# Kernel optimization log

Hardware: AMD Instinct MI355X
Metric: run time of the kernel (lower is better)

## Reference

```python
import jax, jax.numpy as jnp
import numpy as np

N = 50000
E = 200000
DIMS = [3, 64, 64, 64, 128, 1024, 512, 256, 2]  # hard-coded layer widths from __init__


def setup_inputs() -> dict:
    key = jax.random.key(0)
    ks = jax.random.split(key, 2 + 2 * 8)
    inp = {}
    inp["x"] = jax.random.normal(ks[0], (N, DIMS[0]), dtype=jnp.float32)
    inp["edge_index"] = jax.random.randint(ks[1], (2, E), 0, N, dtype=jnp.int32)
    for i in range(8):
        w = jax.random.normal(ks[2 + 2 * i], (DIMS[i], DIMS[i + 1]), dtype=jnp.float32) / np.sqrt(DIMS[i]).astype(np.float32)
        b = jax.random.normal(ks[3 + 2 * i], (DIMS[i + 1],), dtype=jnp.float32) * 0.01
        inp[f"W{i}"] = w
        inp[f"b{i}"] = b
    return inp


def _gcn_layer(x, row, col, norm, W, b, n):
    # PyG GCNConv: h = x @ W; out_i = sum_{j->i} norm_ij * h_j; out += b
    h = x @ W                          # [N, F_out]
    msg = h[row] * norm[:, None]       # [E+N, F_out] gather + scale
    out = jax.ops.segment_sum(msg, col, num_segments=n)  # scatter-add
    return out + b


def reference(x, edge_index, W0, b0, W1, b1, W2, b2, W3, b3, W4, b4, W5, b5, W6, b6, W7, b7):
    n = x.shape[0]
    # add self-loops (GCNConv default add_self_loops=True)
    loops = jnp.arange(n, dtype=edge_index.dtype)
    row = jnp.concatenate([edge_index[0], loops])  # source nodes
    col = jnp.concatenate([edge_index[1], loops])  # target nodes
    # symmetric degree normalization: deg counts incoming edges at col
    deg = jax.ops.segment_sum(jnp.ones_like(col, dtype=x.dtype), col, num_segments=n)
    dis = jnp.where(deg > 0, jax.lax.rsqrt(jnp.maximum(deg, 1e-12)), 0.0)
    norm = dis[row] * dis[col]  # [E+N]

    Ws = [W0, W1, W2, W3, W4, W5, W6, W7]
    bs = [b0, b1, b2, b3, b4, b5, b6, b7]
    # dropout is identity in eval mode (training=False)
    for i in range(7):
        x = jax.nn.relu(_gcn_layer(x, row, col, norm, Ws[i], bs[i], n))
    x = _gcn_layer(x, row, col, norm, Ws[7], bs[7], n)
    return x
```

## Files before the change

### kernel.cpp

```cpp
#include <hip/hip_runtime.h>
#include <hip/hip_bf16.h>

typedef __hip_bfloat16 bf16;
typedef __attribute__((ext_vector_type(8))) short short8;
typedef __attribute__((ext_vector_type(4))) float floatx4;

__device__ inline float ldf(const float* p, size_t i) { return p[i]; }
__device__ inline float ldf(const bf16* p, size_t i) { return (float)p[i]; }
__device__ inline void stf(float* p, size_t i, float v) { p[i] = v; }
__device__ inline void stf(bf16* p, size_t i, float v) { p[i] = (bf16)v; }

__device__ inline void async16(const bf16* g, bf16* l) {
    __builtin_amdgcn_global_load_lds(
        (const __attribute__((address_space(1))) void*)g,
        (__attribute__((address_space(3))) void*)l, 16, 0, 0);
}

__device__ inline void loadvec(const float* __restrict__ p, float* d) {
    float4 v = *(const float4*)p;
    d[0] = v.x; d[1] = v.y; d[2] = v.z; d[3] = v.w;
}
__device__ inline void loadvec(const bf16* __restrict__ p, float* d) {
    uint4 u = *(const uint4*)p;
    const unsigned* w = (const unsigned*)&u;
    #pragma unroll
    for (int j = 0; j < 4; ++j) {
        d[2 * j]     = __uint_as_float(w[j] << 16);
        d[2 * j + 1] = __uint_as_float(w[j] & 0xffff0000u);
    }
}
template <int VEC, typename TOut>
__device__ inline void storevec(TOut* __restrict__ p, const float* d) {
    if constexpr (sizeof(TOut) == 4) {
        #pragma unroll
        for (int j = 0; j < VEC; j += 4) {
            float4 v = {d[j], d[j + 1], d[j + 2], d[j + 3]};
            *(float4*)(p + j) = v;
        }
    } else {
        unsigned w[VEC / 2];
        #pragma unroll
        for (int j = 0; j < VEC / 2; ++j) {
            bf16 lo = (bf16)d[2 * j], hi = (bf16)d[2 * j + 1];
            w[j] = ((unsigned)*(unsigned short*)&hi << 16) | (unsigned)*(unsigned short*)&lo;
        }
        if constexpr (VEC == 8) *(uint4*)p = *(uint4*)&w[0];
        else                    *(uint2*)p = *(uint2*)&w[0];
    }
}

__global__ void detect_dtype_kernel(const unsigned short* __restrict__ x, int* __restrict__ flag) {
    __shared__ float s[256];
    float m = 0.0f;
    for (int i = threadIdx.x; i < 512; i += 256) {
        unsigned int u = ((unsigned int)x[i]) << 16;
        float v = __uint_as_float(u);
        if (!isnan(v)) m = fmaxf(m, fabsf(v));
    }
    s[threadIdx.x] = m;
    __syncthreads();
    for (int o = 128; o > 0; o >>= 1) {
        if (threadIdx.x < (unsigned)o) s[threadIdx.x] = fmaxf(s[threadIdx.x], s[threadIdx.x + o]);
        __syncthreads();
    }
    if (threadIdx.x == 0) flag[0] = (s[0] > 1e3f) ? 0 : 1;
}

struct CvtJobs {
    const void* src[14];
    float* dst[14];
    int off[15];
    int cnt;
};
__global__ void cvt_fused_kernel(CvtJobs j, const int* __restrict__ flag) {
    int t = blockIdx.x * 256 + threadIdx.x;
    if (t >= j.off[j.cnt]) return;
    int k = 0;
    while (t >= j.off[k + 1]) ++k;
    int e = t - j.off[k];
    float v = *flag ? (float)((const bf16*)j.src[k])[e] : ((const float*)j.src[k])[e];
    j.dst[k][e] = v;
}

struct WtJobs {
    const void* src[3];
    bf16* dst[3];
    int K[3], N[3];
    int off[4];
};
__global__ void wt_fused_kernel(WtJobs j, const int* __restrict__ flag) {
    int t = blockIdx.x * 256 + threadIdx.x;
    if (t >= j.off[3]) return;
    int k_ = 0;
    while (t >= j.off[k_ + 1]) ++k_;
    int e = t - j.off[k_];
    int K = j.K[k_], Nn = j.N[k_];
    int n = e / K, kk = e % K;
    size_t si = (size_t)kk * Nn + n;
    float v = *flag ? (float)((const bf16*)j.src[k_])[si] : ((const float*)j.src[k_])[si];
    j.dst[k_][e] = (bf16)v;
}

__global__ void out_kernel(const float* __restrict__ in, void* __restrict__ out,
                           int n, const int* __restrict__ flag) {
    int i = blockIdx.x * blockDim.x + threadIdx.x;
    if (i >= n) return;
    if (*flag) ((bf16*)out)[i] = (bf16)in[i];
    else       ((float*)out)[i] = in[i];
}

__global__ void zero_int_kernel(int* a, int n) {
    int i = blockIdx.x * blockDim.x + threadIdx.x;
    if (i < n) a[i] = 0;
}

__global__ void hist_kernel(const int* __restrict__ col, int* __restrict__ counts, int E) {
    int e = blockIdx.x * blockDim.x + threadIdx.x;
    if (e < E) atomicAdd(&counts[col[e]], 1);
}

__global__ void scan_reduce_kernel(const int* __restrict__ counts, int* __restrict__ bs, int n) {
    __shared__ int s[1024];
    int i = blockIdx.x * 1024 + threadIdx.x;
    s[threadIdx.x] = (i < n) ? counts[i] : 0;
    __syncthreads();
    for (int o = 512; o > 0; o >>= 1) {
        if (threadIdx.x < (unsigned)o) s[threadIdx.x] += s[threadIdx.x + o];
        __syncthreads();
    }
    if (threadIdx.x == 0) bs[blockIdx.x] = s[0];
}

__global__ void scan_blocksums_kernel(int* __restrict__ bs, int nb) {
    __shared__ int s[1024];
    int v = (threadIdx.x < (unsigned)nb) ? bs[threadIdx.x] : 0;
    s[threadIdx.x] = v;
    __syncthreads();
    for (int off = 1; off < 1024; off <<= 1) {
        int t = (threadIdx.x >= (unsigned)off) ? s[threadIdx.x - off] : 0;
        __syncthreads();
        s[threadIdx.x] += t;
        __syncthreads();
    }
    if (threadIdx.x < (unsigned)nb) bs[threadIdx.x] = s[threadIdx.x] - v;
}

__global__ void scan_final_kernel(int* __restrict__ counts, const int* __restrict__ bs,
                                  int* __restrict__ offsets, float* __restrict__ dis, int n) {
    __shared__ int s[1024];
    int i = blockIdx.x * 1024 + threadIdx.x;
    int v = (i < n) ? counts[i] : 0;
    if (i < n) { dis[i] = rsqrtf((float)(v + 1)); counts[i] = 0; }
    s[threadIdx.x] = v;
    __syncthreads();
    for (int off = 1; off < 1024; off <<= 1) {
        int t = (threadIdx.x >= (unsigned)off) ? s[threadIdx.x - off] : 0;
        __syncthreads();
        s[threadIdx.x] += t;
        __syncthreads();
    }
    if (i < n) offsets[i + 1] = s[threadIdx.x] + bs[blockIdx.x];
    if (i == 0) offsets[0] = 0;
}

__global__ void fill_kernel(const int* __restrict__ row, const int* __restrict__ col,
                            const int* __restrict__ offsets, int* __restrict__ cursor,
                            int* __restrict__ csr_src, int E) {
    int e = blockIdx.x * blockDim.x + threadIdx.x;
    if (e < E) {
        int d = col[e];
        int pos = offsets[d] + atomicAdd(&cursor[d], 1);
        csr_src[pos] = row[e];
    }
}

template <typename TIn, typename TOut>
__global__ void agg_kernel(const TIn* __restrict__ h, const int* __restrict__ offsets,
                           const int* __restrict__ csr_src, const float* __restrict__ dis,
                           const float* __restrict__ bias, TOut* __restrict__ out,
                           int n, int F, int add_bias, int relu) {
    long long idx = (long long)blockIdx.x * blockDim.x + threadIdx.x;
    long long total = (long long)n * F;
    if (idx >= total) return;
    int i = (int)(idx / F);
    int f = (int)(idx % F);
    float di = dis[i];
    float acc = di * ldf(h, (size_t)i * F + f);
    int e0 = offsets[i], e1 = offsets[i + 1];
    for (int e = e0; e < e1; ++e) {
        int s = csr_src[e];
        acc += dis[s] * ldf(h, (size_t)s * F + f);
    }
    acc *= di;
    if (add_bias) acc += bias[f];
    if (relu) acc = fmaxf(acc, 0.0f);
    stf(out, (size_t)idx, acc);
}

template <int F, int DO_BIAS, int DO_RELU, typename TIn, typename TOut>
__global__ __launch_bounds__(256) void agg_vec_kernel(
        const TIn* __restrict__ h, const int* __restrict__ offsets,
        const int* __restrict__ csr_src, const float* __restrict__ dis,
        const float* __restrict__ bias, TOut* __restrict__ out, int n) {
    constexpr int VEC = 16 / sizeof(TIn);
    constexpr int CPL = F / VEC;
    int t = blockIdx.x * 256 + threadIdx.x;
    if (t >= n * CPL) return;
    int i = t / CPL;
    int c = t % CPL;
    int fbase = c * VEC;
    float di = dis[i];
    float acc[VEC];
    loadvec(h + (size_t)i * F + fbase, acc);
    #pragma unroll
    for (int v = 0; v < VEC; ++v) acc[v] *= di;
    int e0 = offsets[i], e1 = offsets[i + 1];
    for (int e = e0; e < e1; ++e) {
        int s = csr_src[e];
        float dsv = dis[s];
        float tmp[VEC];
        loadvec(h + (size_t)s * F + fbase, tmp);
        #pragma unroll
        for (int v = 0; v < VEC; ++v) acc[v] += dsv * tmp[v];
    }
    #pragma unroll
    for (int v = 0; v < VEC; ++v) {
        acc[v] *= di;
        if (DO_BIAS) acc[v] += bias[fbase + v];
        if (DO_RELU) acc[v] = fmaxf(acc[v], 0.0f);
    }
    storevec<VEC>(out + (size_t)i * F + fbase, acc);
}

template <typename TIn, typename TOut>
__global__ void gemm_naive_kernel(const TIn* __restrict__ A, const float* __restrict__ W,
                                  const float* __restrict__ bias, TOut* __restrict__ C,
                                  int M, int Nc, int K, int add_bias, int relu) {
    long long idx = (long long)blockIdx.x * blockDim.x + threadIdx.x;
    long long total = (long long)M * Nc;
    if (idx >= total) return;
    int m = (int)(idx / Nc);
    int nc = (int)(idx % Nc);
    float acc = 0.0f;
    for (int k = 0; k < K; ++k)
        acc += ldf(A, (size_t)m * K + k) * W[(size_t)k * Nc + nc];
    if (add_bias) acc += bias[nc];
    if (relu) acc = fmaxf(acc, 0.0f);
    stf(C, (size_t)idx, acc);
}

#define TM 64
#define TN 64
#define TK 16
template <typename TIn, typename TOut>
__global__ __launch_bounds__(256) void gemm_tiled_kernel(
        const TIn* __restrict__ A, const float* __restrict__ W,
        const float* __restrict__ bias, TOut* __restrict__ C,
        int M, int Nc, int K, int add_bias, int relu) {
    __shared__ float As[TK][TM + 1];
    __shared__ float Bs[TK][TN + 1];
    int bm = blockIdx.x * TM;
    int bn = blockIdx.y * TN;
    int tid = threadIdx.x;
    int tm = (tid >> 4) << 2;
    int tn = (tid & 15) << 2;
    float acc[4][4] = {};
    for (int k0 = 0; k0 < K; k0 += TK) {
        #pragma unroll
        for (int l = 0; l < 4; ++l) {
            int idx = tid + l * 256;
            int m = idx >> 4;
            int k = idx & 15;
            int gm = bm + m;
            As[k][m] = (gm < M) ? ldf(A, (size_t)gm * K + k0 + k) : 0.0f;
        }
        #pragma unroll
        for (int l = 0; l < 4; ++l) {
            int idx = tid + l * 256;
            int k = idx >> 6;
            int nn = idx & 63;
            Bs[k][nn] = W[(size_t)(k0 + k) * Nc + bn + nn];
        }
        __syncthreads();
        #pragma unroll
        for (int k = 0; k < TK; ++k) {
            float a[4], b[4];
            #pragma unroll
            for (int i = 0; i < 4; ++i) a[i] = As[k][tm + i];
            #pragma unroll
            for (int j = 0; j < 4; ++j) b[j] = Bs[k][tn + j];
            #pragma unroll
            for (int i = 0; i < 4; ++i)
                #pragma unroll
                for (int j = 0; j < 4; ++j) acc[i][j] += a[i] * b[j];
        }
        __syncthreads();
    }
    #pragma unroll
    for (int i = 0; i < 4; ++i) {
        int gm = bm + tm + i;
        if (gm >= M) continue;
        #pragma unroll
        for (int j = 0; j < 4; ++j) {
            int gn = bn + tn + j;
            float v = acc[i][j];
            if (add_bias) v += bias[gn];
            if (relu) v = fmaxf(v, 0.0f);
            stf(C, (size_t)gm * Nc + gn, v);
        }
    }
}

template <int DO_BIAS, int DO_RELU, typename TOut>
__global__ __launch_bounds__(256) void gemm_mfma_kernel(
        const bf16* __restrict__ A,
        const bf16* __restrict__ Bt,
        const float* __restrict__ bias,
        TOut* __restrict__ C,
        int M, int Nc, int K) {
    __shared__ bf16 As[2][128 * 32];
    __shared__ bf16 Bs[2][128 * 32];
    const int tid  = threadIdx.x;
    const int wave = tid >> 6;
    const int lane = tid & 63;

    const int nwg  = (int)gridDim.x;
    const int orig = (int)blockIdx.x;
    const int q = nwg >> 3, r = nwg & 7;
    const int xcd = orig & 7;
    const int lin = orig >> 3;
    const int swz = (xcd < r ? xcd * (q + 1) : r * (q + 1) + (xcd - r) * q) + lin;
    const int nbn = Nc >> 7;
    const int bm = (swz / nbn) * 128;
    const int bn = (swz % nbn) * 128;

    const int wr = (wave >> 1) * 64;
    const int wc = (wave & 1) * 64;
    const int fm = lane & 15;
    const int fq = lane >> 4;
    const int fk = fq * 8;

    const int e0 = tid * 8;
    const int r0 = e0 >> 5, c0 = e0 & 31;
    const int e1 = (256 + tid) * 8;
    const int r1 = e1 >> 5, c1 = e1 & 31;
    int gmA0 = bm + r0; if (gmA0 > M - 1) gmA0 = M - 1;
    int gmA1 = bm + r1; if (gmA1 > M - 1) gmA1 = M - 1;

    const bf16* a0p = A  + (size_t)gmA0 * K + c0;
    const bf16* a1p = A  + (size_t)gmA1 * K + c1;
    const bf16* b0p = Bt + (size_t)(bn + r0) * K + c0;
    const bf16* b1p = Bt + (size_t)(bn + r1) * K + c1;

    floatx4 acc[4][4] = {};
    const int nt = K >> 5;

    async16(a0p, &As[0][e0]);
    async16(a1p, &As[0][e1]);
    async16(b0p, &Bs[0][e0]);
    async16(b1p, &Bs[0][e1]);

    for (int t = 0; t < nt; ++t) {
        __syncthreads();
        const int cur = t & 1;
        if (t + 1 < nt) {
            const int k0 = (t + 1) << 5;
            async16(a0p + k0, &As[cur ^ 1][e0]);
            async16(a1p + k0, &As[cur ^ 1][e1]);
            async16(b0p + k0, &Bs[cur ^ 1][e0]);
            async16(b1p + k0, &Bs[cur ^ 1][e1]);
        }
        short8 af[4], bfv[4];
        #pragma unroll
        for (int t4 = 0; t4 < 4; ++t4) {
            af[t4]  = *(const short8*)(&As[cur][(wr + t4 * 16 + fm) * 32 + fk]);
            bfv[t4] = *(const short8*)(&Bs[cur][(wc + t4 * 16 + fm) * 32 + fk]);
        }
        #pragma unroll
        for (int mt = 0; mt < 4; ++mt)
            #pragma unroll
            for (int ntc = 0; ntc < 4; ++ntc)
                acc[mt][ntc] = __builtin_amdgcn_mfma_f32_16x16x32_bf16(
                    af[mt], bfv[ntc], acc[mt][ntc], 0, 0, 0);
    }

    #pragma unroll
    for (int mt = 0; mt < 4; ++mt) {
        #pragma unroll
        for (int r2 = 0; r2 < 4; ++r2) {
            int gm = bm + wr + mt * 16 + fq * 4 + r2;
            if (gm >= M) continue;
            #pragma unroll
            for (int ntc = 0; ntc < 4; ++ntc) {
                int gn = bn + wc + ntc * 16 + fm;
                float v = acc[mt][ntc][r2];
                if (DO_BIAS) v += bias[gn];
                if (DO_RELU) v = fmaxf(v, 0.0f);
                stf(C, (size_t)gm * Nc + gn, v);
            }
        }
    }
}


static inline int cdiv(long long a, int b) { return (int)((a + b - 1) / b); }

extern "C" void kernel_launch(void* const* d_in, const int* in_sizes, int n_in,
                              void* d_out, int out_size, void* d_ws, size_t ws_size,
                              hipStream_t stream) {
    const int N = in_sizes[0] / 3;
    const int E = in_sizes[1] / 2;

    const int* edge_index = (const int*)d_in[1];
    const int* row = edge_index;
    const int* col = edge_index + E;

    char* p = (char*)d_ws;
    auto alloc = [&](size_t bytes) {
        void* r = (void*)p;
        p += (bytes + 255) & ~(size_t)255;
        return r;
    };
    void* bufA    = alloc((size_t)N * 2048);
    void* bufB    = alloc((size_t)N * 1024);
    float* dis    = (float*)alloc((size_t)N * sizeof(float));
    int* offsets  = (int*)alloc((size_t)(N + 1) * sizeof(int));
    int* cursor   = (int*)alloc((size_t)N * sizeof(int));
    int* csr_src  = (int*)alloc((size_t)E * sizeof(int));
    int* flag     = (int*)alloc(256);
    int* blocksums = (int*)alloc((size_t)cdiv(N, 1024) * sizeof(int));
    const int WfL[5] = {0, 1, 2, 3, 7};
    float* Wf[8] = {};
    float* bf_[8];
    for (int t = 0; t < 5; ++t) {
        int L = WfL[t];
        Wf[L] = (float*)alloc((size_t)in_sizes[2 + 2 * L] * sizeof(float));
    }
    for (int L = 0; L < 8; ++L)
        bf_[L] = (float*)alloc((size_t)in_sizes[3 + 2 * L] * sizeof(float));
    bf16* Wt4 = (bf16*)alloc((size_t)128 * 1024 * sizeof(bf16));
    bf16* Wt5 = (bf16*)alloc((size_t)1024 * 512 * sizeof(bf16));
    bf16* Wt6 = (bf16*)alloc((size_t)512 * 256 * sizeof(bf16));
    size_t needed = (size_t)(p - (char*)d_ws);
    if (ws_size < needed) return;

    float* fA = (float*)bufA;  bf16* hA = (bf16*)bufA;
    float* fB = (float*)bufB;  bf16* hB = (bf16*)bufB;

    const int T = 256;

    detect_dtype_kernel<<<1, 256, 0, stream>>>((const unsigned short*)d_in[0], flag);

    {
        CvtJobs cj{};
        int idx = 0, cum = 0;
        auto add = [&](const void* s, float* d, int n) {
            cj.src[idx] = s; cj.dst[idx] = d; cj.off[idx] = cum; cum += n; ++idx;
        };
        add(d_in[0], fA, N * 3);
        for (int t = 0; t < 5; ++t) {
            int L = WfL[t];
            add(d_in[2 + 2 * L], Wf[L], in_sizes[2 + 2 * L]);
        }
        for (int L = 0; L < 8; ++L)
            add(d_in[3 + 2 * L], bf_[L], in_sizes[3 + 2 * L]);
        cj.off[idx] = cum; cj.cnt = idx;
        cvt_fused_kernel<<<cdiv(cum, T), T, 0, stream>>>(cj, flag);
    }

    {
        WtJobs wj{};
        wj.src[0] = d_in[2 + 2 * 4]; wj.dst[0] = Wt4; wj.K[0] = 128;  wj.N[0] = 1024;
        wj.src[1] = d_in[2 + 2 * 5]; wj.dst[1] = Wt5; wj.K[1] = 1024; wj.N[1] = 512;
        wj.src[2] = d_in[2 + 2 * 6]; wj.dst[2] = Wt6; wj.K[2] = 512;  wj.N[2] = 256;
        wj.off[0] = 0;
        wj.off[1] = 128 * 1024;
        wj.off[2] = 128 * 1024 + 1024 * 512;
        wj.off[3] = 128 * 1024 + 1024 * 512 + 512 * 256;
        wt_fused_kernel<<<cdiv(wj.off[3], T), T, 0, stream>>>(wj, flag);
    }

    {
        zero_int_kernel<<<cdiv(N, T), T, 0, stream>>>(cursor, N);
        hist_kernel<<<cdiv(E, T), T, 0, stream>>>(col, cursor, E);
        int nb = cdiv(N, 1024);
        scan_reduce_kernel<<<nb, 1024, 0, stream>>>(cursor, blocksums, N);
        scan_blocksums_kernel<<<1, 1024, 0, stream>>>(blocksums, nb);
        scan_final_kernel<<<nb, 1024, 0, stream>>>(cursor, blocksums, offsets, dis, N);
        fill_kernel<<<cdiv(E, T), T, 0, stream>>>(row, col, offsets, cursor, csr_src, E);
    }


    agg_kernel<float, float><<<cdiv((long long)N * 3, T), T, 0, stream>>>(
        fA, offsets, csr_src, dis, nullptr, fB, N, 3, 0, 0);
    gemm_naive_kernel<float, float><<<cdiv((long long)N * 64, T), T, 0, stream>>>(
        fB, Wf[0], bf_[0], fA, N, 64, 3, 1, 1);

    {
        dim3 g(cdiv(N, TM), 64 / TN);
        gemm_tiled_kernel<float, float><<<g, 256, 0, stream>>>(fA, Wf[1], nullptr, fB, N, 64, 64, 0, 0);
        agg_vec_kernel<64, 1, 1, float, float><<<cdiv((long long)N * 16, T), T, 0, stream>>>(
            fB, offsets, csr_src, dis, bf_[1], fA, N);
    }

    {
        dim3 g(cdiv(N, TM), 64 / TN);
        gemm_tiled_kernel<float, float><<<g, 256, 0, stream>>>(fA, Wf[2], nullptr, fB, N, 64, 64, 0, 0);
        agg_vec_kernel<64, 1, 1, float, float><<<cdiv((long long)N * 16, T), T, 0, stream>>>(
            fB, offsets, csr_src, dis, bf_[2], fA, N);
    }

    {
        agg_vec_kernel<64, 0, 0, float, float><<<cdiv((long long)N * 16, T), T, 0, stream>>>(
            fA, offsets, csr_src, dis, nullptr, fB, N);
        dim3 g(cdiv(N, TM), 128 / TN);
        gemm_tiled_kernel<float, bf16><<<g, 256, 0, stream>>>(fB, Wf[3], bf_[3], hA, N, 128, 64, 1, 1);
    }

    {
        agg_vec_kernel<128, 0, 0, bf16, bf16><<<cdiv((long long)N * 16, T), T, 0, stream>>>(
            hA, offsets, csr_src, dis, nullptr, hB, N);
        int nwg = cdiv(N, 128) * (1024 / 128);
        gemm_mfma_kernel<1, 1, bf16><<<nwg, 256, 0, stream>>>(hB, Wt4, bf_[4], hA, N, 1024, 128);
    }

    {
        int nwg = cdiv(N, 128) * (512 / 128);
        gemm_mfma_kernel<0, 0, bf16><<<nwg, 256, 0, stream>>>(hA, Wt5, nullptr, hB, N, 512, 1024);
        agg_vec_kernel<512, 1, 1, bf16, bf16><<<cdiv((long long)N * 64, T), T, 0, stream>>>(
            hB, offsets, csr_src, dis, bf_[5], hA, N);
    }

    {
        int nwg = cdiv(N, 128) * (256 / 128);
        gemm_mfma_kernel<0, 0, bf16><<<nwg, 256, 0, stream>>>(hA, Wt6, nullptr, hB, N, 256, 512);
        agg_vec_kernel<256, 1, 1, bf16, bf16><<<cdiv((long long)N * 32, T), T, 0, stream>>>(
            hB, offsets, csr_src, dis, bf_[6], hA, N);
    }

    {
        gemm_naive_kernel<bf16, float><<<cdiv((long long)N * 2, T), T, 0, stream>>>(
            hA, Wf[7], nullptr, fB, N, 2, 256, 0, 0);
        agg_kernel<float, float><<<cdiv((long long)N * 2, T), T, 0, stream>>>(
            fB, offsets, csr_src, dis, bf_[7], fA, N, 2, 1, 0);
    }

    out_kernel<<<cdiv((long long)N * 2, T), T, 0, stream>>>(fA, d_out, N * 2, flag);
}
```

Measured before the change: 565.9 us.

## Triple-buffer MFMA GEMM LDS tiles and XOR-swizzle layout to avoid bank conflicts

```diff
diff --git a/kernel.cpp b/kernel.cpp
--- a/kernel.cpp
+++ b/kernel.cpp
@@ -318,8 +318,8 @@
         const float* __restrict__ bias,
         TOut* __restrict__ C,
         int M, int Nc, int K) {
-    __shared__ bf16 As[2][128 * 32];
-    __shared__ bf16 Bs[2][128 * 32];
+    __shared__ bf16 As[3][128 * 32];
+    __shared__ bf16 Bs[3][128 * 32];
     const int tid  = threadIdx.x;
     const int wave = tid >> 6;
     const int lane = tid & 63;
@@ -338,43 +338,50 @@
     const int wc = (wave & 1) * 64;
     const int fm = lane & 15;
     const int fq = lane >> 4;
-    const int fk = fq * 8;
-
+    const int fks = (fq ^ ((fm >> 1) & 3)) << 3;
+
+    const int r0 = tid >> 2;
+    const int r1 = (256 + tid) >> 2;
+    const int sc0 = ((tid & 3) ^ ((r0 >> 1) & 3)) << 3;
+    const int sc1 = (((256 + tid) & 3) ^ ((r1 >> 1) & 3)) << 3;
     const int e0 = tid * 8;
-    const int r0 = e0 >> 5, c0 = e0 & 31;
     const int e1 = (256 + tid) * 8;
-    const int r1 = e1 >> 5, c1 = e1 & 31;
     int gmA0 = bm + r0; if (gmA0 > M - 1) gmA0 = M - 1;
     int gmA1 = bm + r1; if (gmA1 > M - 1) gmA1 = M - 1;
 
-    const bf16* a0p = A  + (size_t)gmA0 * K + c0;
-    const bf16* a1p = A  + (size_t)gmA1 * K + c1;
-    const bf16* b0p = Bt + (size_t)(bn + r0) * K + c0;
-    const bf16* b1p = Bt + (size_t)(bn + r1) * K + c1;
+    const bf16* a0p = A  + (size_t)gmA0 * K + sc0;
+    const bf16* a1p = A  + (size_t)gmA1 * K + sc1;
+    const bf16* b0p = Bt + (size_t)(bn + r0) * K + sc0;
+    const bf16* b1p = Bt + (size_t)(bn + r1) * K + sc1;
+
+    auto stage = [&](int slot, int kt) {
+        const int k0 = kt << 5;
+        async16(a0p + k0, &As[slot][e0]);
+        async16(a1p + k0, &As[slot][e1]);
+        async16(b0p + k0, &Bs[slot][e0]);
+        async16(b1p + k0, &Bs[slot][e1]);
+    };
 
     floatx4 acc[4][4] = {};
     const int nt = K >> 5;
 
-    async16(a0p, &As[0][e0]);
-    async16(a1p, &As[0][e1]);
-    async16(b0p, &Bs[0][e0]);
-    async16(b1p, &Bs[0][e1]);
-
+    stage(0, 0);
+    if (nt > 1) stage(1, 1);
+
+    int cur = 0;
     for (int t = 0; t < nt; ++t) {
-        __syncthreads();
-        const int cur = t & 1;
-        if (t + 1 < nt) {
-            const int k0 = (t + 1) << 5;
-            async16(a0p + k0, &As[cur ^ 1][e0]);
-            async16(a1p + k0, &As[cur ^ 1][e1]);
-            async16(b0p + k0, &Bs[cur ^ 1][e0]);
-            async16(b1p + k0, &Bs[cur ^ 1][e1]);
+        if (t + 1 < nt) asm volatile("s_waitcnt vmcnt(4)" ::: "memory");
+        else            asm volatile("s_waitcnt vmcnt(0)" ::: "memory");
+        __builtin_amdgcn_s_barrier();
+        if (t + 2 < nt) {
+            int sp = cur + 2; if (sp >= 3) sp -= 3;
+            stage(sp, t + 2);
         }
         short8 af[4], bfv[4];
         #pragma unroll
         for (int t4 = 0; t4 < 4; ++t4) {
-            af[t4]  = *(const short8*)(&As[cur][(wr + t4 * 16 + fm) * 32 + fk]);
-            bfv[t4] = *(const short8*)(&Bs[cur][(wc + t4 * 16 + fm) * 32 + fk]);
+            af[t4]  = *(const short8*)(&As[cur][(wr + t4 * 16 + fm) * 32 + fks]);
+            bfv[t4] = *(const short8*)(&Bs[cur][(wc + t4 * 16 + fm) * 32 + fks]);
         }
         #pragma unroll
         for (int mt = 0; mt < 4; ++mt)
@@ -382,13 +389,14 @@
             for (int ntc = 0; ntc < 4; ++ntc)
                 acc[mt][ntc] = __builtin_amdgcn_mfma_f32_16x16x32_bf16(
                     af[mt], bfv[ntc], acc[mt][ntc], 0, 0, 0);
+        ++cur; if (cur >= 3) cur = 0;
     }
 
     #pragma unroll
     for (int mt = 0; mt < 4; ++mt) {
         #pragma unroll
         for (int r2 = 0; r2 < 4; ++r2) {
-            int gm = bm + wr + mt * 16 + fq * 4 + r2;
+            int gm = bm + wr + mt * 16 + (lane >> 4) * 4 + r2;
             if (gm >= M) continue;
             #pragma unroll
             for (int ntc = 0; ntc < 4; ++ntc) {
```

Result: no change. 568.5 us (+0.5%).
